# Performance work log

Measured on AMD Instinct MI355X. Metric: run time of the kernel, lower is better.

The kernel has to match this reference:

```python
import jax, jax.numpy as jnp
import numpy as np

NC, TOP_K, ALPHA, BETA, EPS = 80, 13, 1.0, 6.0, 1e-9
IMG = 640


def _make_anchors():
    pts = []
    for stride in (8, 16, 32):
        n = IMG // stride
        c = (np.arange(n, dtype=np.float32) + 0.5) * stride
        yy, xx = np.meshgrid(c, c, indexing='ij')
        pts.append(np.stack([xx.ravel(), yy.ravel()], axis=-1))
    return jnp.asarray(np.concatenate(pts, axis=0))  # (8400, 2)


def setup_inputs() -> dict:
    key = jax.random.key(0)
    ks = jax.random.split(key, 8)
    b, n_max = 32, 32
    anchor_points = _make_anchors()
    A = anchor_points.shape[0]
    pred_scores = jax.random.uniform(ks[0], (b, A, NC), dtype=jnp.float32)
    # predicted boxes: centers near anchors, sizes in [8, 72]
    ctr = anchor_points[None] + 5.0 * jax.random.normal(ks[1], (b, A, 2), dtype=jnp.float32)
    wh = 8.0 + 64.0 * jax.random.uniform(ks[2], (b, A, 2), dtype=jnp.float32)
    pred_bboxes = jnp.concatenate([ctr - wh / 2, ctr + wh / 2], axis=-1)
    # gt boxes: random centers in image, sizes in [20, 180]
    gctr = IMG * jax.random.uniform(ks[3], (b, n_max, 2), dtype=jnp.float32)
    gwh = 20.0 + 160.0 * jax.random.uniform(ks[4], (b, n_max, 2), dtype=jnp.float32)
    gt_bboxes = jnp.concatenate([gctr - gwh / 2, gctr + gwh / 2], axis=-1)
    gt_labels = jax.random.randint(ks[5], (b, n_max, 1), 0, NC, dtype=jnp.int64)
    n_valid = jax.random.randint(ks[6], (b,), 1, n_max + 1)
    mask_gt = (jnp.arange(n_max)[None, :] < n_valid[:, None]).astype(jnp.float32)[..., None]
    return {
        'pred_scores': pred_scores, 'pred_bboxes': pred_bboxes,
        'anchor_points': anchor_points, 'gt_labels': gt_labels,
        'gt_bboxes': gt_bboxes, 'mask_gt': mask_gt,
    }


def _iou_pairwise(gt, pd, eps=1e-7):
    # gt: (b,n,1,4), pd: (b,1,A,4) -> (b,n,A) elementwise-broadcast IoU
    lt = jnp.maximum(gt[..., :2], pd[..., :2])
    rb = jnp.minimum(gt[..., 2:], pd[..., 2:])
    inter = jnp.clip(rb - lt, 0).prod(-1)
    area_g = (gt[..., 2:] - gt[..., :2]).prod(-1)
    area_p = (pd[..., 2:] - pd[..., :2]).prod(-1)
    return inter / (area_g + area_p - inter + eps)


def reference(pred_scores, pred_bboxes, anchor_points, gt_labels, gt_bboxes, mask_gt):
    b, A, nc = pred_scores.shape
    n = gt_bboxes.shape[1]
    dt = pred_scores.dtype
    mg = mask_gt[..., 0] > 0  # (b,n) valid-gt mask

    # --- candidates whose anchor center lies inside the gt box ---
    lt, rb = gt_bboxes[:, :, None, :2], gt_bboxes[:, :, None, 2:]
    deltas = jnp.concatenate([anchor_points[None, None] - lt, rb - anchor_points[None, None]], axis=-1)
    mask_in_gts = deltas.min(-1) > EPS  # (b,n,A)
    valid = mask_in_gts & mg[:, :, None]

    # --- box metrics: class score gathered at gt label, IoU(gt, pred) ---
    lbl = jnp.clip(gt_labels[..., 0], 0, nc - 1)  # (b,n)
    ps = jnp.swapaxes(pred_scores, 1, 2)  # (b,nc,A)
    bbox_scores = jnp.take_along_axis(ps, lbl[:, :, None], axis=1)  # (b,n,A)
    bbox_scores = jnp.where(valid, bbox_scores, jnp.zeros((), dt))
    overlaps = jnp.clip(_iou_pairwise(gt_bboxes[:, :, None], pred_bboxes[:, None]), 0)
    overlaps = jnp.where(valid, overlaps, jnp.zeros((), dt))
    align_metric = bbox_scores ** ALPHA * overlaps ** BETA  # (b,n,A)

    # --- top-k candidate selection (duplicate indices zeroed, as in torch) ---
    _, idx = jax.lax.top_k(align_metric, TOP_K)  # (b,n,K)
    idx = jnp.where(mg[:, :, None], idx, 0)
    rows = jnp.arange(b * n)[:, None]
    counts = jnp.zeros((b * n, A), jnp.int32).at[rows, idx.reshape(b * n, TOP_K)].add(1)
    counts = counts.reshape(b, n, A)
    mask_topk = jnp.where(counts > 1, 0, counts).astype(dt)
    mask_pos = mask_topk * valid.astype(dt)  # (b,n,A)

    # --- resolve anchors assigned to multiple gts: keep highest IoU ---
    fg = mask_pos.sum(1)  # (b,A)
    is_max = jnp.swapaxes(jax.nn.one_hot(overlaps.argmax(1), n, dtype=dt), 1, 2)  # (b,n,A)
    mask_pos = jnp.where(fg[:, None, :] > 1, is_max, mask_pos)
    fg = mask_pos.sum(1)

    # --- gather targets ---
    tgi = mask_pos.argmax(1)  # (b,A)
    t_labels = jnp.take_along_axis(lbl, tgi, axis=1)  # (b,A), already >= 0
    target_bboxes = jnp.take_along_axis(gt_bboxes, tgi[:, :, None], axis=1)  # (b,A,4)
    target_scores = jax.nn.one_hot(t_labels, nc, dtype=dt)
    target_scores = jnp.where(fg[:, :, None] > 0, target_scores, jnp.zeros((), dt))

    # --- normalize scores by alignment metric ---
    am = align_metric * mask_pos
    pos_align = am.max(-1, keepdims=True)  # (b,n,1)
    pos_ov = (overlaps * mask_pos).max(-1, keepdims=True)
    norm = (am * pos_ov / (pos_align + EPS)).max(1)[:, :, None]  # (b,A,1)
    target_scores = target_scores * norm
    return target_bboxes, target_scores, fg > 0
```

## Files before the change

### kernel.cpp

```cpp
#include <hip/hip_runtime.h>

#define B_CNT 32
#define N_CNT 32
#define A_CNT 8400
#define NC_CNT 80
#define TOPK 13
#define CAND_CAP 1024
#define EPS_IN 1e-9f

typedef unsigned long long u64;
typedef unsigned int u32;


__global__ void __launch_bounds__(256) k1(const float* __restrict__ ps,
        const float* __restrict__ pb, const float* __restrict__ ap,
        const int* __restrict__ gl, const float* __restrict__ gb,
        const float* __restrict__ mgt,
        int* __restrict__ cIdx, float* __restrict__ cAl, float* __restrict__ cOv) {
    __shared__ u64 cand[CAND_CAP];
    __shared__ int cnt;
    int bn = blockIdx.x;
    int b = bn >> 5;
    int tid = threadIdx.x;
    bool mg = mgt[bn] > 0.f;
    if (!mg) {
        if (tid < TOPK) {
            cIdx[bn * TOPK + tid] = -1;
            cAl [bn * TOPK + tid] = 0.f;
            cOv [bn * TOPK + tid] = 0.f;
        }
        return;
    }
    float4 g = ((const float4*)gb)[bn];
    int lbl = min(max(gl[bn], 0), NC_CNT - 1);
    float area_g = (g.z - g.x) * (g.w - g.y);
    const float*  psb = ps + (size_t)b * A_CNT * NC_CNT;
    const float4* pbb = (const float4*)(pb + (size_t)b * A_CNT * 4);
    const float2* ap2 = (const float2*)ap;

    if (tid == 0) cnt = 0;
    __syncthreads();

    for (int a = tid; a < A_CNT; a += 256) {
        float2 aq = ap2[a];
        float dmin = fminf(fminf(aq.x - g.x, aq.y - g.y), fminf(g.z - aq.x, g.w - aq.y));
        if (dmin > EPS_IN) {
            float4 p = pbb[a];
            float ix = fminf(g.z, p.z) - fmaxf(g.x, p.x);
            float iy = fminf(g.w, p.w) - fmaxf(g.y, p.y);
            float inter = fmaxf(ix, 0.f) * fmaxf(iy, 0.f);
            float area_p = (p.z - p.x) * (p.w - p.y);
            float ov = inter / (area_g + area_p - inter + 1e-7f);
            ov = fmaxf(ov, 0.f);
            float sc = psb[(size_t)a * NC_CNT + lbl];
            float o2 = ov * ov;
            float al = sc * (o2 * o2 * o2);
            if (al > 0.f) {
                int slot = atomicAdd(&cnt, 1);
                if (slot < CAND_CAP)
                    cand[slot] = ((u64)__float_as_uint(al) << 32) | (u64)(0xFFFFFFFFu - (u32)a);
            }
        }
    }
    __syncthreads();
    if (tid >= 64) return;

    int nc = min(cnt, CAND_CAP);
    u64 keys[16];
#pragma unroll
    for (int j = 0; j < 16; j++) {
        int s = j * 64 + tid;
        keys[j] = (s < nc) ? cand[s] : 0;
    }

    u64 myw = 0;
    for (int pass = 0; pass < TOPK; ++pass) {
        u64 m = keys[0];
#pragma unroll
        for (int j = 1; j < 16; j++) if (keys[j] > m) m = keys[j];
#pragma unroll
        for (int off = 1; off <= 32; off <<= 1) {
            u64 o = __shfl_xor(m, off);
            if (o > m) m = o;
        }
        if (pass == tid) myw = m;
#pragma unroll
        for (int j = 0; j < 16; j++) if (keys[j] == m) keys[j] = 0;
    }

    if (tid < TOPK) {
        u64 w = myw;
        int ci = -1; float al = 0.f, ov = 0.f;
        if (w != 0) {
            int i = (int)(0xFFFFFFFFu - (u32)(w & 0xFFFFFFFFull));
            al = __uint_as_float((u32)(w >> 32));
            float4 p = pbb[i];
            float ix = fminf(g.z, p.z) - fmaxf(g.x, p.x);
            float iy = fminf(g.w, p.w) - fmaxf(g.y, p.y);
            float inter = fmaxf(ix, 0.f) * fmaxf(iy, 0.f);
            float area_p = (p.z - p.x) * (p.w - p.y);
            ov = inter / (area_g + area_p - inter + 1e-7f);
            ov = fmaxf(ov, 0.f);
            ci = i;
        }
        cIdx[bn * TOPK + tid] = ci;
        cAl [bn * TOPK + tid] = al;
        cOv [bn * TOPK + tid] = ov;
    }
}

__global__ void __launch_bounds__(448) k2(const float* __restrict__ ps,
        const float* __restrict__ pb, const float* __restrict__ ap,
        const int* __restrict__ gl, const float* __restrict__ gb,
        const float* __restrict__ mgt,
        const int* __restrict__ cIdx, const float* __restrict__ cAl, const float* __restrict__ cOv,
        int* __restrict__ tgi, float* __restrict__ alT, float* __restrict__ fgw,
        int* __restrict__ posAl, int* __restrict__ posOv) {
    __shared__ int   sIdx[N_CNT][TOPK];
    __shared__ float sAl[N_CNT][TOPK];
    __shared__ float sOv[N_CNT][TOPK];
    __shared__ float4 gs[N_CNT];
    __shared__ float  mgs[N_CNT];
    __shared__ int    lbls[N_CNT];
    int b = blockIdx.x;
    int tid = threadIdx.x;
    if (tid < N_CNT) {
        int bn = b * N_CNT + tid;
        gs[tid]   = ((const float4*)gb)[bn];
        mgs[tid]  = mgt[bn];
        lbls[tid] = min(max(gl[bn], 0), NC_CNT - 1);
    }
    for (int t = tid; t < N_CNT * TOPK; t += 448) {
        int r = t / TOPK, k = t - r * TOPK;
        int src = b * N_CNT * TOPK + t;
        sIdx[r][k] = cIdx[src];
        sAl [r][k] = cAl [src];
        sOv [r][k] = cOv [src];
    }
    __syncthreads();
    if (tid >= N_CNT * TOPK) return;
    int n = tid / TOPK, k = tid - n * TOPK;
    int i = sIdx[n][k];
    if (i < 0) return;

    unsigned int m = 0;
    for (int nn = 0; nn < N_CNT; nn++) {
        bool has = false;
#pragma unroll
        for (int kk = 0; kk < TOPK; kk++) has = has || (sIdx[nn][kk] == i);
        m |= (has ? 1u : 0u) << nn;
    }
    int fg = __popc(m);
    int first = __ffs(m) - 1;
    if (n != first) return;

    size_t ba = (size_t)b * A_CNT + i;
    int t; float al, ovw;
    if (fg == 1) {
        t = n; al = sAl[n][k]; ovw = sOv[n][k];
    } else {
        float2 aq = ((const float2*)ap)[i];
        float4 p = ((const float4*)pb)[ba];
        float area_p = (p.z - p.x) * (p.w - p.y);
        float bo = -1.f; int bt = 0;
        for (int nn = 0; nn < N_CNT; nn++) {
            float4 g = gs[nn];
            float dmin = fminf(fminf(aq.x - g.x, aq.y - g.y), fminf(g.z - aq.x, g.w - aq.y));
            bool v = (mgs[nn] > 0.f) && (dmin > EPS_IN);
            float ov = 0.f;
            if (v) {
                float ix = fminf(g.z, p.z) - fmaxf(g.x, p.x);
                float iy = fminf(g.w, p.w) - fmaxf(g.y, p.y);
                float inter = fmaxf(ix, 0.f) * fmaxf(iy, 0.f);
                float area_g = (g.z - g.x) * (g.w - g.y);
                ov = inter / (area_g + area_p - inter + 1e-7f);
                ov = fmaxf(ov, 0.f);
            }
            if (ov > bo) { bo = ov; bt = nn; }
        }
        t = bt;
        float sc = ps[ba * NC_CNT + lbls[t]];
        float o2 = bo * bo;
        al = sc * (o2 * o2 * o2);
        ovw = bo;
    }
    int lw = b * N_CNT + t;
    tgi[ba] = t;
    alT[ba] = al;
    fgw[ba] = 1.f;
    atomicMax(&posAl[lw], __float_as_int(al));
    atomicMax(&posOv[lw], __float_as_int(ovw));
}

__global__ void __launch_bounds__(256) k3(const int* __restrict__ tgi, const float* __restrict__ alT,
        const float* __restrict__ fgw, const int* __restrict__ posAl, const int* __restrict__ posOv,
        const int* __restrict__ gl, const float* __restrict__ gb,
        float* __restrict__ out_bbox, float* __restrict__ out_scores, float* __restrict__ out_fg) {
    int idx = blockIdx.x * 256 + threadIdx.x;
    if (idx >= B_CNT * A_CNT * (NC_CNT / 4)) return;
    int ba = idx / 20;
    int q  = idx - ba * 20;
    int b  = ba / A_CNT;
    int t  = tgi[ba];
    int bn = b * N_CNT + t;
    float fgv = fgw[ba];
    float norm = 0.f;
    if (fgv > 0.f) {
        float pa = __int_as_float(posAl[bn]);
        float po = __int_as_float(posOv[bn]);
        norm = alT[ba] * po / (pa + 1e-9f);
    }
    int lbl = min(max(gl[bn], 0), NC_CNT - 1);
    int c0 = q * 4;
    float4 v;
    v.x = (fgv > 0.f && lbl == c0    ) ? norm : 0.f;
    v.y = (fgv > 0.f && lbl == c0 + 1) ? norm : 0.f;
    v.z = (fgv > 0.f && lbl == c0 + 2) ? norm : 0.f;
    v.w = (fgv > 0.f && lbl == c0 + 3) ? norm : 0.f;
    ((float4*)out_scores)[idx] = v;
    if (q == 0) {
        ((float4*)out_bbox)[ba] = ((const float4*)gb)[bn];
        out_fg[ba] = fgv;
    }
}

extern "C" void kernel_launch(void* const* d_in, const int* in_sizes, int n_in,
                              void* d_out, int out_size, void* d_ws, size_t ws_size,
                              hipStream_t stream) {
    const float* pred_scores   = (const float*)d_in[0];
    const float* pred_bboxes   = (const float*)d_in[1];
    const float* anchor_points = (const float*)d_in[2];
    const int*   gt_labels     = (const int*)d_in[3];
    const float* gt_bboxes     = (const float*)d_in[4];
    const float* mask_gt       = (const float*)d_in[5];

    const int BA = B_CNT * A_CNT;
    const int BN = B_CNT * N_CNT;

    char* w = (char*)d_ws;
    int*   posAl   = (int*)w;                  w += (size_t)BN * 4;
    int*   posOv   = (int*)w;                  w += (size_t)BN * 4;
    int*   tgi     = (int*)w;                  w += (size_t)BA * 4;
    float* alT     = (float*)w;                w += (size_t)BA * 4;
    float* fgw     = (float*)w;                w += (size_t)BA * 4;
    int*   cIdx    = (int*)w;                  w += (size_t)BN * TOPK * 4;
    float* cAl     = (float*)w;                w += (size_t)BN * TOPK * 4;
    float* cOv     = (float*)w;                w += (size_t)BN * TOPK * 4;

    float* out_bbox   = (float*)d_out;
    float* out_scores = out_bbox + (size_t)BA * 4;
    float* out_fg     = out_scores + (size_t)BA * NC_CNT;

    hipMemsetAsync(posAl, 0, ((size_t)2 * BN + (size_t)3 * BA) * 4, stream);

    k1<<<dim3(BN), dim3(256), 0, stream>>>(pred_scores, pred_bboxes, anchor_points,
                                           gt_labels, gt_bboxes, mask_gt,
                                           cIdx, cAl, cOv);
    k2<<<dim3(B_CNT), dim3(448), 0, stream>>>(pred_scores, pred_bboxes, anchor_points,
                                              gt_labels, gt_bboxes, mask_gt,
                                              cIdx, cAl, cOv,
                                              tgi, alT, fgw, posAl, posOv);
    k3<<<dim3((BA * (NC_CNT / 4) + 255) / 256), dim3(256), 0, stream>>>(tgi, alT, fgw,
                                              posAl, posOv, gt_labels, gt_bboxes,
                                              out_bbox, out_scores, out_fg);
}
```

Baseline: 209.4 us.

## Restrict k1 anchor scan to grid cells overlapping each gt box

k1 no longer loops over all 8400 anchors for each (batch, gt) block. It computes, per stride level, the range of grid cells that overlap the gt box and visits only those, rebuilding anchor coordinates arithmetically instead of loading anchor_points. Extra sentinel candidates for the first 13 anchors are added so the top-k fallback matches the reference's tie behaviour when few anchors score positive, and the final pass re-checks whether each selected anchor lies inside the box. This removes most global loads and compute in k1, at the cost of index arithmetic and more complex tie-handling logic.

```diff
diff --git a/kernel.cpp b/kernel.cpp
--- a/kernel.cpp
+++ b/kernel.cpp
@@ -12,8 +12,9 @@
 typedef unsigned int u32;
 
 
+
 __global__ void __launch_bounds__(256) k1(const float* __restrict__ ps,
-        const float* __restrict__ pb, const float* __restrict__ ap,
+        const float* __restrict__ pb,
         const int* __restrict__ gl, const float* __restrict__ gb,
         const float* __restrict__ mgt,
         int* __restrict__ cIdx, float* __restrict__ cAl, float* __restrict__ cOv) {
@@ -36,19 +37,46 @@
     float area_g = (g.z - g.x) * (g.w - g.y);
     const float*  psb = ps + (size_t)b * A_CNT * NC_CNT;
     const float4* pbb = (const float4*)(pb + (size_t)b * A_CNT * 4);
-    const float2* ap2 = (const float2*)ap;
 
     if (tid == 0) cnt = 0;
     __syncthreads();
 
-    for (int a = tid; a < A_CNT; a += 256) {
-        float2 aq = ap2[a];
-        float dmin = fminf(fminf(aq.x - g.x, aq.y - g.y), fminf(g.z - aq.x, g.w - aq.y));
+    const int   dims[3]  = {80, 40, 20};
+    const int   bases[3] = {0, 6400, 8000};
+    const float sfs[3]   = {8.f, 16.f, 32.f};
+    int xlo[3], ylo[3], wds[3], cells[3];
+    int T = 0;
+    for (int s = 0; s < 3; s++) {
+        float inv = 1.f / sfs[s];
+        int ix0 = max(0, (int)floorf(g.x * inv - 0.5f) - 1);
+        int ix1 = min(dims[s] - 1, (int)floorf(g.z * inv - 0.5f) + 1);
+        int iy0 = max(0, (int)floorf(g.y * inv - 0.5f) - 1);
+        int iy1 = min(dims[s] - 1, (int)floorf(g.w * inv - 0.5f) + 1);
+        int w = ix1 - ix0 + 1, h = iy1 - iy0 + 1;
+        if (w < 0) w = 0;
+        if (h < 0) h = 0;
+        xlo[s] = ix0; ylo[s] = iy0; wds[s] = w;
+        cells[s] = w * h;
+        T += cells[s];
+    }
+
+    for (int t = tid; t < T; t += 256) {
+        int s = 0, r = t;
+        if (r >= cells[0]) { r -= cells[0]; s = 1; }
+        if (s == 1 && r >= cells[1]) { r -= cells[1]; s = 2; }
+        int w = wds[s];
+        int iy = ylo[s] + r / w;
+        int ix = xlo[s] + r - (r / w) * w;
+        float sf = sfs[s];
+        float ax = ((float)ix + 0.5f) * sf;
+        float ay = ((float)iy + 0.5f) * sf;
+        float dmin = fminf(fminf(ax - g.x, ay - g.y), fminf(g.z - ax, g.w - ay));
         if (dmin > EPS_IN) {
+            int a = bases[s] + iy * dims[s] + ix;
             float4 p = pbb[a];
-            float ix = fminf(g.z, p.z) - fmaxf(g.x, p.x);
-            float iy = fminf(g.w, p.w) - fmaxf(g.y, p.y);
-            float inter = fmaxf(ix, 0.f) * fmaxf(iy, 0.f);
+            float ixx = fminf(g.z, p.z) - fmaxf(g.x, p.x);
+            float iyy = fminf(g.w, p.w) - fmaxf(g.y, p.y);
+            float inter = fmaxf(ixx, 0.f) * fmaxf(iyy, 0.f);
             float area_p = (p.z - p.x) * (p.w - p.y);
             float ov = inter / (area_g + area_p - inter + 1e-7f);
             ov = fmaxf(ov, 0.f);
@@ -62,6 +90,31 @@
             }
         }
     }
+
+    if (tid < TOPK) {
+        int j = tid;
+        float ax = ((float)j + 0.5f) * 8.f;
+        float ay = 4.f;
+        float dmin = fminf(fminf(ax - g.x, ay - g.y), fminf(g.z - ax, g.w - ay));
+        bool dup = false;
+        if (dmin > EPS_IN) {
+            float4 p = pbb[j];
+            float ixx = fminf(g.z, p.z) - fmaxf(g.x, p.x);
+            float iyy = fminf(g.w, p.w) - fmaxf(g.y, p.y);
+            float inter = fmaxf(ixx, 0.f) * fmaxf(iyy, 0.f);
+            float area_p = (p.z - p.x) * (p.w - p.y);
+            float ov = inter / (area_g + area_p - inter + 1e-7f);
+            ov = fmaxf(ov, 0.f);
+            float sc = psb[(size_t)j * NC_CNT + lbl];
+            float o2 = ov * ov;
+            dup = (sc * (o2 * o2 * o2)) > 0.f;
+        }
+        if (!dup) {
+            int slot = atomicAdd(&cnt, 1);
+            if (slot < CAND_CAP)
+                cand[slot] = (u64)(0xFFFFFFFFu - (u32)j);
+        }
+    }
     __syncthreads();
     if (tid >= 64) return;
 
@@ -94,14 +147,27 @@
         if (w != 0) {
             int i = (int)(0xFFFFFFFFu - (u32)(w & 0xFFFFFFFFull));
             al = __uint_as_float((u32)(w >> 32));
-            float4 p = pbb[i];
-            float ix = fminf(g.z, p.z) - fmaxf(g.x, p.x);
-            float iy = fminf(g.w, p.w) - fmaxf(g.y, p.y);
-            float inter = fmaxf(ix, 0.f) * fmaxf(iy, 0.f);
-            float area_p = (p.z - p.x) * (p.w - p.y);
-            ov = inter / (area_g + area_p - inter + 1e-7f);
-            ov = fmaxf(ov, 0.f);
-            ci = i;
+            int s = (i < 6400) ? 0 : ((i < 8000) ? 1 : 2);
+            const int   dims2[3]  = {80, 40, 20};
+            const int   bases2[3] = {0, 6400, 8000};
+            const float sfs2[3]   = {8.f, 16.f, 32.f};
+            int r = i - bases2[s];
+            int iy = r / dims2[s], ix = r - iy * dims2[s];
+            float ax = ((float)ix + 0.5f) * sfs2[s];
+            float ay = ((float)iy + 0.5f) * sfs2[s];
+            float dmin = fminf(fminf(ax - g.x, ay - g.y), fminf(g.z - ax, g.w - ay));
+            if (dmin > EPS_IN) {
+                float4 p = pbb[i];
+                float ixx = fminf(g.z, p.z) - fmaxf(g.x, p.x);
+                float iyy = fminf(g.w, p.w) - fmaxf(g.y, p.y);
+                float inter = fmaxf(ixx, 0.f) * fmaxf(iyy, 0.f);
+                float area_p = (p.z - p.x) * (p.w - p.y);
+                ov = inter / (area_g + area_p - inter + 1e-7f);
+                ov = fmaxf(ov, 0.f);
+                ci = i;
+            } else {
+                al = 0.f;
+            }
         }
         cIdx[bn * TOPK + tid] = ci;
         cAl [bn * TOPK + tid] = al;
@@ -253,7 +319,7 @@
 
     hipMemsetAsync(posAl, 0, ((size_t)2 * BN + (size_t)3 * BA) * 4, stream);
 
-    k1<<<dim3(BN), dim3(256), 0, stream>>>(pred_scores, pred_bboxes, anchor_points,
+    k1<<<dim3(BN), dim3(256), 0, stream>>>(pred_scores, pred_bboxes,
                                            gt_labels, gt_bboxes, mask_gt,
                                            cIdx, cAl, cOv);
     k2<<<dim3(B_CNT), dim3(448), 0, stream>>>(pred_scores, pred_bboxes, anchor_points,
```

After: 195.6 us. -6.6%, faster.
